# Performance work log

Measured on AMD Instinct MI355X. Metric: run time of the kernel, lower is better.

## Reference

```python
import jax, jax.numpy as jnp
import numpy as np

D_MODEL = 1024
NUM_HEADS = 16
D_K = D_MODEL // NUM_HEADS


def setup_inputs() -> dict:
    key = jax.random.key(0)
    ks = jax.random.split(key, 9)
    B, S = 2, 2048
    scale = 1.0 / np.sqrt(D_MODEL)
    x = jax.random.normal(ks[0], (B, S, D_MODEL), dtype=jnp.float32)
    Wq = jax.random.normal(ks[1], (D_MODEL, D_MODEL), dtype=jnp.float32) * scale
    Wk = jax.random.normal(ks[2], (D_MODEL, D_MODEL), dtype=jnp.float32) * scale
    Wv = jax.random.normal(ks[3], (D_MODEL, D_MODEL), dtype=jnp.float32) * scale
    Wo = jax.random.normal(ks[4], (D_MODEL, D_MODEL), dtype=jnp.float32) * scale
    bq = jax.random.normal(ks[5], (D_MODEL,), dtype=jnp.float32) * 0.01
    bk = jax.random.normal(ks[6], (D_MODEL,), dtype=jnp.float32) * 0.01
    bv = jax.random.normal(ks[7], (D_MODEL,), dtype=jnp.float32) * 0.01
    bo = jax.random.normal(ks[8], (D_MODEL,), dtype=jnp.float32) * 0.01
    return {"x": x, "Wq": Wq, "bq": bq, "Wk": Wk, "bk": bk,
            "Wv": Wv, "bv": bv, "Wo": Wo, "bo": bo}


def reference(x, Wq, bq, Wk, bk, Wv, bv, Wo, bo):
    B, S, _ = x.shape
    H, Dk = NUM_HEADS, D_K
    # projections -> [B, H, S, Dk]
    def split_heads(t):
        return t.reshape(B, S, H, Dk).transpose(0, 2, 1, 3)
    q = split_heads(x @ Wq + bq)
    k = split_heads(x @ Wk + bk)
    v = split_heads(x @ Wv + bv)
    # full score matrix [B, H, S, S] (faithful to the original non-fused impl)
    scores = jnp.einsum('bhqd,bhkd->bhqk', q, k) / jnp.sqrt(jnp.float32(Dk))
    attn = jax.nn.softmax(scores, axis=-1)
    out = jnp.einsum('bhqk,bhkd->bhqd', attn, v)
    out = out.transpose(0, 2, 1, 3).reshape(B, S, H * Dk)
    return out @ Wo + bo
```

## Files before the change

### kernel.cpp

```cpp
#include <hip/hip_runtime.h>
#include <cstdint>

constexpr int S    = 2048;
constexpr int D    = 1024;
constexpr int NH   = 16;
constexpr int DK   = 64;
constexpr int MTOK = 2 * S;

typedef __bf16 bf16x8 __attribute__((ext_vector_type(8)));
typedef __bf16 bf16x4 __attribute__((ext_vector_type(4)));
typedef float  floatx4 __attribute__((ext_vector_type(4)));

__device__ __forceinline__ void async_cp16(const void* g, void* l) {
    __builtin_amdgcn_global_load_lds(
        (const __attribute__((address_space(1))) uint32_t*)g,
        (__attribute__((address_space(3))) uint32_t*)l, 16, 0, 0);
}

__global__ __launch_bounds__(256) void cvt_bf16(const float* __restrict__ in,
                                                __bf16* __restrict__ out, int n) {
    int i = (blockIdx.x * 256 + threadIdx.x) * 4;
    if (i + 3 < n) {
        float4 v = *(const float4*)&in[i];
        bf16x4 o;
        o[0] = (__bf16)v.x; o[1] = (__bf16)v.y; o[2] = (__bf16)v.z; o[3] = (__bf16)v.w;
        *(bf16x4*)&out[i] = o;
    }
}

__global__ __launch_bounds__(256) void cvt_transpose_w(
    const float* __restrict__ W0, const float* __restrict__ W1,
    const float* __restrict__ W2, const float* __restrict__ W3,
    __bf16* __restrict__ T0, __bf16* __restrict__ T1,
    __bf16* __restrict__ T2, __bf16* __restrict__ T3)
{
    const float* W = (blockIdx.z == 0) ? W0 : (blockIdx.z == 1) ? W1 : (blockIdx.z == 2) ? W2 : W3;
    __bf16*      T = (blockIdx.z == 0) ? T0 : (blockIdx.z == 1) ? T1 : (blockIdx.z == 2) ? T2 : T3;
    __shared__ __bf16 tile[64][65];
    const int t  = threadIdx.x;
    const int k0 = blockIdx.y * 64, n0 = blockIdx.x * 64;
    #pragma unroll
    for (int i = 0; i < 4; ++i) {
        int k = (t >> 4) + i * 16;
        int n = (t & 15) * 4;
        float4 v = *(const float4*)&W[(size_t)(k0 + k) * D + n0 + n];
        tile[n + 0][k] = (__bf16)v.x;
        tile[n + 1][k] = (__bf16)v.y;
        tile[n + 2][k] = (__bf16)v.z;
        tile[n + 3][k] = (__bf16)v.w;
    }
    __syncthreads();
    #pragma unroll
    for (int i = 0; i < 4; ++i) {
        int n = (t >> 4) + i * 16;
        int k = (t & 15) * 4;
        bf16x4 o;
        o[0] = tile[n][k]; o[1] = tile[n][k + 1]; o[2] = tile[n][k + 2]; o[3] = tile[n][k + 3];
        *(bf16x4*)&T[(size_t)(n0 + n) * D + k0 + k] = o;
    }
}

constexpr int BM = 128, BK = 64;

template<int JT>
__device__ __forceinline__ void gemm_core(
    const __bf16* __restrict__ A, const __bf16* __restrict__ Bt,
    __bf16* Alds, __bf16* Blds, int m0, int n0, floatx4 (&acc)[4][JT])
{
    const int tid = threadIdx.x;
    const int w = tid >> 6, l = tid & 63;
    const int wm = (w >> 1) * 64, wn = (w & 1) * 16 * JT;
    const int lr = l & 15, lg = l >> 4;

    #pragma unroll
    for (int i = 0; i < 4; ++i)
        #pragma unroll
        for (int j = 0; j < JT; ++j)
            acc[i][j] = (floatx4){0.f, 0.f, 0.f, 0.f};

    for (int k0 = 0; k0 < D; k0 += BK) {
        #pragma unroll
        for (int i = 0; i < 4; ++i) {
            int c = i * 256 + tid, row = c >> 3, g = c & 7;
            async_cp16(&A[(size_t)(m0 + row) * D + k0 + g * 8], &Alds[c * 8]);
        }
        #pragma unroll
        for (int i = 0; i < JT; ++i) {
            int c = i * 256 + tid, row = c >> 3, g = c & 7;
            async_cp16(&Bt[(size_t)(n0 + row) * D + k0 + g * 8], &Blds[c * 8]);
        }
        __syncthreads();
        #pragma unroll
        for (int kk = 0; kk < 2; ++kk) {
            bf16x8 af[4], bfr[JT];
            #pragma unroll
            for (int i = 0; i < 4; ++i)
                af[i] = *(const bf16x8*)&Alds[(wm + i * 16 + lr) * BK + kk * 32 + lg * 8];
            #pragma unroll
            for (int j = 0; j < JT; ++j)
                bfr[j] = *(const bf16x8*)&Blds[(wn + j * 16 + lr) * BK + kk * 32 + lg * 8];
            #pragma unroll
            for (int i = 0; i < 4; ++i)
                #pragma unroll
                for (int j = 0; j < JT; ++j)
                    acc[i][j] = __builtin_amdgcn_mfma_f32_16x16x32_bf16(af[i], bfr[j], acc[i][j], 0, 0, 0);
        }
        __syncthreads();
    }
}

__global__ __launch_bounds__(256, 2) void gemm_qkv(
    const __bf16* __restrict__ xb,
    const __bf16* __restrict__ WqT, const __bf16* __restrict__ WkT, const __bf16* __restrict__ WvT,
    const float* __restrict__ bq, const float* __restrict__ bk, const float* __restrict__ bv,
    __bf16* __restrict__ Qb, __bf16* __restrict__ Kb, __bf16* __restrict__ Vt)
{
    __shared__ __align__(16) __bf16 Alds[BM * BK];
    __shared__ __align__(16) __bf16 Blds[128 * BK];
    const int z = blockIdx.z;
    const __bf16* Bt   = (z == 0) ? WqT : (z == 1) ? WkT : WvT;
    const float*  bias = (z == 0) ? bq : (z == 1) ? bk : bv;
    const float   scale = (z == 0) ? 0.125f : 1.0f;
    const int m0 = blockIdx.y * BM, n0 = blockIdx.x * 128;

    floatx4 acc[4][4];
    gemm_core<4>(xb, Bt, Alds, Blds, m0, n0, acc);

    const int tid = threadIdx.x;
    const int w = tid >> 6, l = tid & 63;
    const int wm = (w >> 1) * 64, wn = (w & 1) * 64;
    const int lr = l & 15, lg = l >> 4;

    if (z < 2) {
        __bf16* Out = (z == 0) ? Qb : Kb;
        #pragma unroll
        for (int i = 0; i < 4; ++i)
            #pragma unroll
            for (int j = 0; j < 4; ++j) {
                int n = n0 + wn + j * 16 + lr;
                #pragma unroll
                for (int r = 0; r < 4; ++r) {
                    int m = m0 + wm + i * 16 + lg * 4 + r;
                    float v = (acc[i][j][r] + bias[n]) * scale;
                    size_t off = ((size_t)((m >> 11) * NH + (n >> 6)) * S + (m & (S - 1))) * DK + (n & (DK - 1));
                    Out[off] = (__bf16)v;
                }
            }
    } else {
        #pragma unroll
        for (int i = 0; i < 4; ++i)
            #pragma unroll
            for (int j = 0; j < 4; ++j) {
                int n = n0 + wn + j * 16 + lr;
                int m = m0 + wm + i * 16 + lg * 4;
                float bn = bias[n];
                bf16x4 o;
                #pragma unroll
                for (int r = 0; r < 4; ++r) o[r] = (__bf16)(acc[i][j][r] + bn);
                size_t off = ((size_t)((m >> 11) * NH + (n >> 6)) * DK + (n & (DK - 1))) * S + (m & (S - 1));
                *(bf16x4*)&Vt[off] = o;
            }
    }
}

__global__ __launch_bounds__(256, 2) void gemm_out(
    const __bf16* __restrict__ A, const __bf16* __restrict__ Bt,
    const float* __restrict__ bias, float* __restrict__ Cout)
{
    __shared__ __align__(16) __bf16 Alds[BM * BK];
    __shared__ __align__(16) __bf16 Blds[64 * BK];
    const int m0 = blockIdx.y * BM, n0 = blockIdx.x * 64;

    floatx4 acc[4][2];
    gemm_core<2>(A, Bt, Alds, Blds, m0, n0, acc);

    const int tid = threadIdx.x;
    const int w = tid >> 6, l = tid & 63;
    const int wm = (w >> 1) * 64, wn = (w & 1) * 32;
    const int lr = l & 15, lg = l >> 4;
    #pragma unroll
    for (int i = 0; i < 4; ++i)
        #pragma unroll
        for (int j = 0; j < 2; ++j) {
            int n = n0 + wn + j * 16 + lr;
            #pragma unroll
            for (int r = 0; r < 4; ++r) {
                int m = m0 + wm + i * 16 + lg * 4 + r;
                Cout[(size_t)m * D + n] = acc[i][j][r] + bias[n];
            }
        }
}

constexpr int QT = 128;
constexpr int KT = 64;
constexpr float SOFTMAX_C = 10.0f;

__global__ __launch_bounds__(256, 2) void attn_mfma(
    const __bf16* __restrict__ Q, const __bf16* __restrict__ K,
    const __bf16* __restrict__ Vt, __bf16* __restrict__ O)
{
    __shared__ __align__(16) __bf16 Klds[2][KT * DK];
    __shared__ __align__(16) __bf16 Vlds[2][DK * KT];
    __shared__ __align__(16) __bf16 Plds[4][32 * 64];

    const int tid = threadIdx.x;
    const int w = tid >> 6, l = tid & 63;
    const int lr = l & 15, lg = l >> 4;
    const int bh = blockIdx.y;
    const int q0 = blockIdx.x * QT;
    const __bf16* Kbase = K  + (size_t)bh * S * DK;
    const __bf16* Vbase = Vt + (size_t)bh * DK * S;

    bf16x8 qf[2][2];
    {
        const __bf16* qp = Q + ((size_t)bh * S + q0 + w * 32) * DK;
        #pragma unroll
        for (int i = 0; i < 2; ++i)
            #pragma unroll
            for (int kk = 0; kk < 2; ++kk)
                qf[i][kk] = *(const bf16x8*)&qp[(i * 16 + lr) * DK + kk * 32 + lg * 8];
    }

    floatx4 acc[4][2];
    #pragma unroll
    for (int jd = 0; jd < 4; ++jd)
        #pragma unroll
        for (int i = 0; i < 2; ++i)
            acc[jd][i] = (floatx4){0.f, 0.f, 0.f, 0.f};
    float psum[2] = {0.f, 0.f};

    auto stage = [&](int buf, int t0) {
        #pragma unroll
        for (int ii = 0; ii < 2; ++ii) {
            int c = ii * 256 + tid;
            int row = c >> 3, c8 = c & 7;
            async_cp16(&Kbase[(size_t)(t0 + row) * DK + c8 * 8], &Klds[buf][c * 8]);
            async_cp16(&Vbase[(size_t)row * S + t0 + c8 * 8],    &Vlds[buf][c * 8]);
        }
    };

    stage(0, 0);

    for (int t0 = 0; t0 < S; t0 += KT) {
        const int cur = (t0 >> 6) & 1;
        __syncthreads();
        if (t0 + KT < S) stage(cur ^ 1, t0 + KT);

        floatx4 sa[4][2];
        #pragma unroll
        for (int j = 0; j < 4; ++j)
            #pragma unroll
            for (int i = 0; i < 2; ++i)
                sa[j][i] = (floatx4){0.f, 0.f, 0.f, 0.f};
        #pragma unroll
        for (int kk = 0; kk < 2; ++kk) {
            bf16x8 kf[4];
            #pragma unroll
            for (int j = 0; j < 4; ++j)
                kf[j] = *(const bf16x8*)&Klds[cur][(j * 16 + lr) * DK + kk * 32 + lg * 8];
            #pragma unroll
            for (int j = 0; j < 4; ++j)
                #pragma unroll
                for (int i = 0; i < 2; ++i)
                    sa[j][i] = __builtin_amdgcn_mfma_f32_16x16x32_bf16(kf[j], qf[i][kk], sa[j][i], 0, 0, 0);
        }

        #pragma unroll
        for (int j = 0; j < 4; ++j)
            #pragma unroll
            for (int i = 0; i < 2; ++i) {
                floatx4 p;
                #pragma unroll
                for (int r = 0; r < 4; ++r) p[r] = __expf(sa[j][i][r] - SOFTMAX_C);
                psum[i] += (p[0] + p[1]) + (p[2] + p[3]);
                bf16x4 pb;
                #pragma unroll
                for (int r = 0; r < 4; ++r) pb[r] = (__bf16)p[r];
                int gsw = (j * 2 + (lg >> 1)) ^ (lr & 7);
                *(bf16x4*)&Plds[w][(i * 16 + lr) * 64 + gsw * 8 + (lg & 1) * 4] = pb;
            }

        #pragma unroll
        for (int kk = 0; kk < 2; ++kk) {
            bf16x8 vf[4], pf[2];
            #pragma unroll
            for (int i = 0; i < 2; ++i) {
                int gsw = (kk * 4 + lg) ^ (lr & 7);
                pf[i] = *(const bf16x8*)&Plds[w][(i * 16 + lr) * 64 + gsw * 8];
            }
            #pragma unroll
            for (int jd = 0; jd < 4; ++jd)
                vf[jd] = *(const bf16x8*)&Vlds[cur][(jd * 16 + lr) * KT + kk * 32 + lg * 8];
            #pragma unroll
            for (int jd = 0; jd < 4; ++jd)
                #pragma unroll
                for (int i = 0; i < 2; ++i)
                    acc[jd][i] = __builtin_amdgcn_mfma_f32_16x16x32_bf16(vf[jd], pf[i], acc[jd][i], 0, 0, 0);
        }
    }

    float inv[2];
    #pragma unroll
    for (int i = 0; i < 2; ++i) {
        float v = psum[i];
        v += __shfl_xor(v, 16);
        v += __shfl_xor(v, 32);
        inv[i] = 1.f / v;
    }
    const int b = bh >> 4, h = bh & 15;
    #pragma unroll
    for (int i = 0; i < 2; ++i) {
        int q = q0 + w * 32 + i * 16 + lr;
        __bf16* op = O + (size_t)(b * S + q) * D + h * DK;
        #pragma unroll
        for (int jd = 0; jd < 4; ++jd) {
            bf16x4 ov;
            #pragma unroll
            for (int r = 0; r < 4; ++r) ov[r] = (__bf16)(acc[jd][i][r] * inv[i]);
            *(bf16x4*)&op[jd * 16 + lg * 4] = ov;
        }
    }
}

extern "C" void kernel_launch(void* const* d_in, const int* in_sizes, int n_in,
                              void* d_out, int out_size, void* d_ws, size_t ws_size,
                              hipStream_t stream) {
    const float* x  = (const float*)d_in[0];
    const float* Wq = (const float*)d_in[1];
    const float* bq = (const float*)d_in[2];
    const float* Wk = (const float*)d_in[3];
    const float* bk = (const float*)d_in[4];
    const float* Wv = (const float*)d_in[5];
    const float* bv = (const float*)d_in[6];
    const float* Wo = (const float*)d_in[7];
    const float* bo = (const float*)d_in[8];

    char* ws = (char*)d_ws;
    __bf16* xb  = (__bf16*)(ws);
    __bf16* WqT = (__bf16*)(ws + (8ull  << 20));
    __bf16* WkT = (__bf16*)(ws + (10ull << 20));
    __bf16* WvT = (__bf16*)(ws + (12ull << 20));
    __bf16* WoT = (__bf16*)(ws + (14ull << 20));
    __bf16* Qb  = (__bf16*)(ws + (16ull << 20));
    __bf16* Kb  = (__bf16*)(ws + (24ull << 20));
    __bf16* Vt  = (__bf16*)(ws + (32ull << 20));
    __bf16* Ob  = (__bf16*)(ws + (40ull << 20));

    cvt_bf16<<<(MTOK * D) / (256 * 4), 256, 0, stream>>>(x, xb, MTOK * D);
    cvt_transpose_w<<<dim3(16, 16, 4), 256, 0, stream>>>(Wq, Wk, Wv, Wo, WqT, WkT, WvT, WoT);

    gemm_qkv<<<dim3(D / 128, MTOK / BM, 3), 256, 0, stream>>>(
        xb, WqT, WkT, WvT, bq, bk, bv, Qb, Kb, Vt);

    attn_mfma<<<dim3(S / QT, 2 * NH), 256, 0, stream>>>(Qb, Kb, Vt, Ob);

    gemm_out<<<dim3(D / 64, MTOK / BM), 256, 0, stream>>>(Ob, WoT, bo, (float*)d_out);
}
```

Measured before the change: 211.8 us.

## Stage K/V through registers with XOR-swizzled LDS layout in attention

```diff
diff --git a/kernel.cpp b/kernel.cpp
--- a/kernel.cpp
+++ b/kernel.cpp
@@ -206,6 +206,7 @@
     const int tid = threadIdx.x;
     const int w = tid >> 6, l = tid & 63;
     const int lr = l & 15, lg = l >> 4;
+    const int sw = lr & 7;
     const int bh = blockIdx.y;
     const int q0 = blockIdx.x * QT;
     const __bf16* Kbase = K  + (size_t)bh * S * DK;
@@ -229,22 +230,31 @@
             acc[jd][i] = (floatx4){0.f, 0.f, 0.f, 0.f};
     float psum[2] = {0.f, 0.f};
 
-    auto stage = [&](int buf, int t0) {
+    bf16x8 kreg[2], vreg[2];
+    auto gload = [&](int t0) {
         #pragma unroll
         for (int ii = 0; ii < 2; ++ii) {
-            int c = ii * 256 + tid;
-            int row = c >> 3, c8 = c & 7;
-            async_cp16(&Kbase[(size_t)(t0 + row) * DK + c8 * 8], &Klds[buf][c * 8]);
-            async_cp16(&Vbase[(size_t)row * S + t0 + c8 * 8],    &Vlds[buf][c * 8]);
+            int c = ii * 256 + tid, row = c >> 3, g = c & 7;
+            kreg[ii] = *(const bf16x8*)&Kbase[(size_t)(t0 + row) * DK + g * 8];
+            vreg[ii] = *(const bf16x8*)&Vbase[(size_t)row * S + t0 + g * 8];
         }
     };
-
-    stage(0, 0);
+    auto lwrite = [&](int buf) {
+        #pragma unroll
+        for (int ii = 0; ii < 2; ++ii) {
+            int c = ii * 256 + tid, row = c >> 3, gs = (c & 7) ^ (row & 7);
+            *(bf16x8*)&Klds[buf][row * 64 + gs * 8] = kreg[ii];
+            *(bf16x8*)&Vlds[buf][row * 64 + gs * 8] = vreg[ii];
+        }
+    };
+
+    gload(0);
+    lwrite(0);
+    gload(KT);
 
     for (int t0 = 0; t0 < S; t0 += KT) {
         const int cur = (t0 >> 6) & 1;
         __syncthreads();
-        if (t0 + KT < S) stage(cur ^ 1, t0 + KT);
 
         floatx4 sa[4][2];
         #pragma unroll
@@ -257,7 +267,7 @@
             bf16x8 kf[4];
             #pragma unroll
             for (int j = 0; j < 4; ++j)
-                kf[j] = *(const bf16x8*)&Klds[cur][(j * 16 + lr) * DK + kk * 32 + lg * 8];
+                kf[j] = *(const bf16x8*)&Klds[cur][(j * 16 + lr) * DK + (((kk * 4 + lg) ^ sw) * 8)];
             #pragma unroll
             for (int j = 0; j < 4; ++j)
                 #pragma unroll
@@ -276,7 +286,7 @@
                 bf16x4 pb;
                 #pragma unroll
                 for (int r = 0; r < 4; ++r) pb[r] = (__bf16)p[r];
-                int gsw = (j * 2 + (lg >> 1)) ^ (lr & 7);
+                int gsw = (j * 2 + (lg >> 1)) ^ sw;
                 *(bf16x4*)&Plds[w][(i * 16 + lr) * 64 + gsw * 8 + (lg & 1) * 4] = pb;
             }
 
@@ -285,17 +295,22 @@
             bf16x8 vf[4], pf[2];
             #pragma unroll
             for (int i = 0; i < 2; ++i) {
-                int gsw = (kk * 4 + lg) ^ (lr & 7);
+                int gsw = (kk * 4 + lg) ^ sw;
                 pf[i] = *(const bf16x8*)&Plds[w][(i * 16 + lr) * 64 + gsw * 8];
             }
             #pragma unroll
             for (int jd = 0; jd < 4; ++jd)
-                vf[jd] = *(const bf16x8*)&Vlds[cur][(jd * 16 + lr) * KT + kk * 32 + lg * 8];
+                vf[jd] = *(const bf16x8*)&Vlds[cur][(jd * 16 + lr) * KT + (((kk * 4 + lg) ^ sw) * 8)];
             #pragma unroll
             for (int jd = 0; jd < 4; ++jd)
                 #pragma unroll
                 for (int i = 0; i < 2; ++i)
                     acc[jd][i] = __builtin_amdgcn_mfma_f32_16x16x32_bf16(vf[jd], pf[i], acc[jd][i], 0, 0, 0);
+        }
+
+        if (t0 + KT < S) {
+            lwrite(cur ^ 1);
+            if (t0 + 2 * KT < S) gload(t0 + 2 * KT);
         }
     }
 
```

Result: faster. 198.2 us (-6.5%).
